# Performance work log

Hardware: AMD Instinct MI355X
Metric: run time of the kernel (lower is better)

Reference implementation:

```python
import jax, jax.numpy as jnp
import numpy as np


def setup_inputs() -> dict:
    key = jax.random.key(0)
    k1, k2 = jax.random.split(key)
    B, S, N, M = 4, 4, 4096, 4096
    output_points = jax.random.normal(k1, (B, S, N, 3), dtype=jnp.float32)
    target_points = jax.random.normal(k2, (B, S, M, 3), dtype=jnp.float32)
    return {"output_points": output_points, "target_points": target_points, "n_samples": 4096}


def reference(output_points, target_points, n_samples):
    # output_points: [B,S,N,3], target_points: [B,S,M,3] (already sampled to n_samples pts)
    x2 = jnp.sum(output_points * output_points, axis=-1)  # [B,S,N]
    y2 = jnp.sum(target_points * target_points, axis=-1)  # [B,S,M]
    xy = jnp.einsum('bsnd,bsmd->bsnm', output_points, target_points)  # [B,S,N,M]
    # squared pairwise distances; clamp tiny negatives from fp error
    d2 = jnp.maximum(x2[..., :, None] + y2[..., None, :] - 2.0 * xy, 0.0)
    dist1 = jnp.min(d2, axis=-1)  # [B,S,N] NN dist output->target (squared)
    dist2 = jnp.min(d2, axis=-2)  # [B,S,M] NN dist target->output (squared)
    # dist_combined per (b,s) = mean(dist1) + mean(dist2); tensor is [S,B]
    chamfer = jnp.mean(dist1, axis=-1) + jnp.mean(dist2, axis=-1)  # [B,S]
    return chamfer.T  # [n_future_steps, batch_size]
```

## Files before the change

### kernel.cpp

```cpp
#include <hip/hip_runtime.h>


constexpr int B = 4, S = 4, NPTS = 4096, PAIRS = B * S;
constexpr int UNITS = PAIRS * 2;
constexpr int THREADS = 512;
constexpr int WAVES = THREADS / 64;
constexpr int AFRAGS = 8;
constexpr int QPB = WAVES * AFRAGS * 16;
constexpr int QCH = NPTS / QPB;
constexpr int RCH = 4;
constexpr int RPB = NPTS / RCH;
constexpr int RTILES = RPB / 16;
constexpr unsigned short BF16_ONE = 0x3F80;

typedef __attribute__((ext_vector_type(8))) short bf16x8;
typedef __attribute__((ext_vector_type(4))) float f32x4;
typedef __attribute__((ext_vector_type(4))) unsigned int u32x4;

static __device__ inline unsigned short bf16_rne(float v) {
  unsigned int u = __builtin_bit_cast(unsigned int, v);
  u += 0x7FFFu + ((u >> 16) & 1u);
  return (unsigned short)(u >> 16);
}
static __device__ inline float bf16f(unsigned short h) {
  unsigned int u = (unsigned int)h << 16;
  return __builtin_bit_cast(float, u);
}
static __device__ inline unsigned int bpack(unsigned short lo, unsigned short hi) {
  return (unsigned int)lo | ((unsigned int)hi << 16);
}

struct Split3 { unsigned short h, m, l; };
static __device__ inline Split3 split3(float v) {
  Split3 s;
  s.h = bf16_rne(v);
  float r = v - bf16f(s.h);
  s.m = bf16_rne(r);
  r -= bf16f(s.m);
  s.l = bf16_rne(r);
  return s;
}


__global__ __launch_bounds__(THREADS, 4)
void chamfer_mfma_main(const float* __restrict__ out_pts,
                       const float* __restrict__ tgt_pts,
                       float* __restrict__ part) {
  const int t = threadIdx.x;
  const int l = t & 63;
  const int wid = t >> 6;
  const int qc = blockIdx.x;
  const int rc = blockIdx.y;
  const int unit = blockIdx.z;
  const int pair = unit >> 1, dir = unit & 1;

  const float* qpts = (dir == 0 ? out_pts : tgt_pts) + (size_t)pair * NPTS * 3;
  const float* rpts = (dir == 0 ? tgt_pts : out_pts) + (size_t)pair * NPTS * 3;

  __shared__ u32x4 lds[RTILES * 64];

  {
    const int q0 = qc * QPB;
    #pragma unroll
    for (int rep = 0; rep < QPB / THREADS; ++rep) {
      const int j = t + rep * THREADS;
      const float x = qpts[3 * (q0 + j)];
      const float y = qpts[3 * (q0 + j) + 1];
      const float z = qpts[3 * (q0 + j) + 2];
      const Split3 sx = split3(x), sy = split3(y), sz = split3(z);
      u32x4* base = lds + (j >> 4) * 64 + (j & 15);
      const u32x4 g0 = {bpack(sx.h, sx.h), bpack(sx.m, sx.h),
                        bpack(sx.l, sx.m), bpack(sy.h, sy.h)};
      const u32x4 g1 = {bpack(sy.m, sy.h), bpack(sy.l, sy.m),
                        bpack(sz.h, sz.h), bpack(sz.m, sz.h)};
      const u32x4 g2 = {bpack(sz.l, sz.m), bpack(BF16_ONE, BF16_ONE),
                        bpack(BF16_ONE, 0), 0u};
      const u32x4 g3 = {0u, 0u, 0u, 0u};
      base[0] = g0; base[16] = g1; base[32] = g2; base[48] = g3;
    }
  }
  __syncthreads();

  bf16x8 a[AFRAGS];
  #pragma unroll
  for (int m = 0; m < AFRAGS; ++m)
    a[m] = ((const bf16x8*)lds)[(wid * AFRAGS + m) * 64 + l];
  __syncthreads();

  {
    const int r0 = rc * RPB;
    #pragma unroll
    for (int rep = 0; rep < RPB / THREADS; ++rep) {
      const int j = t + rep * THREADS;
      const float x = rpts[3 * (r0 + j)];
      const float y = rpts[3 * (r0 + j) + 1];
      const float z = rpts[3 * (r0 + j) + 2];
      const float w = -0.5f * (x * x + y * y + z * z);
      const Split3 sx = split3(x), sy = split3(y), sz = split3(z), sw = split3(w);
      u32x4* base = lds + (j >> 4) * 64 + (j & 15);
      const u32x4 g0 = {bpack(sx.h, sx.m), bpack(sx.h, sx.l),
                        bpack(sx.h, sx.m), bpack(sy.h, sy.m)};
      const u32x4 g1 = {bpack(sy.h, sy.l), bpack(sy.h, sy.m),
                        bpack(sz.h, sz.m), bpack(sz.h, sz.l)};
      const u32x4 g2 = {bpack(sz.h, sz.m), bpack(sw.h, sw.m),
                        bpack(sw.l, 0), 0u};
      const u32x4 g3 = {0u, 0u, 0u, 0u};
      base[0] = g0; base[16] = g1; base[32] = g2; base[48] = g3;
    }
  }
  __syncthreads();

  f32x4 acc[AFRAGS];
  #pragma unroll
  for (int m = 0; m < AFRAGS; ++m)
    acc[m] = (f32x4){-3.0e38f, -3.0e38f, -3.0e38f, -3.0e38f};

  const f32x4 czero = {0.f, 0.f, 0.f, 0.f};
  const bf16x8* bptr = (const bf16x8*)lds;
  for (int tt = 0; tt < RTILES; tt += 2) {
    const bf16x8 b0 = bptr[tt * 64 + l];
    const bf16x8 b1 = bptr[(tt + 1) * 64 + l];
    #pragma unroll
    for (int m = 0; m < AFRAGS; ++m) {
      const f32x4 d0 = __builtin_amdgcn_mfma_f32_16x16x32_bf16(a[m], b0, czero, 0, 0, 0);
      const f32x4 d1 = __builtin_amdgcn_mfma_f32_16x16x32_bf16(a[m], b1, czero, 0, 0, 0);
      #pragma unroll
      for (int c = 0; c < 4; ++c)
        acc[m][c] = fmaxf(fmaxf(acc[m][c], d0[c]), d1[c]);
    }
  }

  #pragma unroll
  for (int m = 0; m < AFRAGS; ++m) {
    #pragma unroll
    for (int c = 0; c < 4; ++c) {
      float g = acc[m][c];
      g = fmaxf(g, __shfl_xor(g, 1, 64));
      g = fmaxf(g, __shfl_xor(g, 2, 64));
      g = fmaxf(g, __shfl_xor(g, 4, 64));
      g = fmaxf(g, __shfl_xor(g, 8, 64));
      acc[m][c] = g;
    }
  }
  const int jj = l & 15, hi = l >> 4;
  float v_lo = 0.f, v_hi = 0.f;
  #pragma unroll
  for (int m = 0; m < 4; ++m) {
    #pragma unroll
    for (int c = 0; c < 4; ++c) {
      const bool sel = (jj == m * 4 + c);
      v_lo = sel ? acc[m][c] : v_lo;
      v_hi = sel ? acc[m + 4][c] : v_hi;
    }
  }
  const int q = qc * QPB + wid * (AFRAGS * 16) + (jj >> 2) * 16 + hi * 4 + (jj & 3);
  float* pdst = part + ((size_t)unit * NPTS + q) * RCH + rc;
  pdst[0] = v_lo;
  pdst[64 * RCH] = v_hi;
}

__global__ __launch_bounds__(256)
void chamfer_finalize(const float* __restrict__ out_pts,
                      const float* __restrict__ tgt_pts,
                      const float* __restrict__ part,
                      float* __restrict__ out) {
  const int t = threadIdx.x;
  const int blk = blockIdx.x;
  const int unit = blk >> 4;
  const int q = (blk & 15) * 256 + t;
  const int pair = unit >> 1, dir = unit & 1;
  const float* qpts = (dir == 0 ? out_pts : tgt_pts) + (size_t)pair * NPTS * 3;

  const f32x4 p = *(const f32x4*)(part + ((size_t)unit * NPTS + q) * RCH);
  const float g = fmaxf(fmaxf(p[0], p[1]), fmaxf(p[2], p[3]));
  const float x = qpts[3 * q], y = qpts[3 * q + 1], z = qpts[3 * q + 2];
  const float x2 = x * x + y * y + z * z;
  float d = fmaxf(fmaf(-2.0f, g, x2), 0.0f);

  #pragma unroll
  for (int off = 1; off < 64; off <<= 1) d += __shfl_xor(d, off, 64);
  __shared__ float sum4[4];
  if ((t & 63) == 0) sum4[t >> 6] = d;
  __syncthreads();
  if (t == 0) {
    const float ssum = (sum4[0] + sum4[1]) + (sum4[2] + sum4[3]);
    const int b = pair >> 2, s = pair & 3;
    atomicAdd(&out[s * B + b], ssum * (1.0f / NPTS));
  }
}

extern "C" void kernel_launch(void* const* d_in, const int* in_sizes, int n_in,
                              void* d_out, int out_size, void* d_ws, size_t ws_size,
                              hipStream_t stream) {
  (void)in_sizes; (void)n_in; (void)ws_size;
  const float* out_pts = (const float*)d_in[0];
  const float* tgt_pts = (const float*)d_in[1];
  float* out = (float*)d_out;
  float* part = (float*)d_ws;

  hipMemsetAsync(out, 0, out_size * sizeof(float), stream);
  dim3 grid(QCH, RCH, UNITS);
  chamfer_mfma_main<<<grid, THREADS, 0, stream>>>(out_pts, tgt_pts, part);
  chamfer_finalize<<<dim3(UNITS * 16), 256, 0, stream>>>(out_pts, tgt_pts, part, out);
}
```

Measured before the change: 92.34 us.

## Fuse finalize into main chamfer kernel with in-block reference loop and prefetch

Result: faster. 87.10 us (-5.7%).

```diff
diff --git a/kernel.cpp b/kernel.cpp
--- a/kernel.cpp
+++ b/kernel.cpp
@@ -1,16 +1,13 @@
 #include <hip/hip_runtime.h>
 
 
-constexpr int B = 4, S = 4, NPTS = 4096, PAIRS = B * S;
-constexpr int UNITS = PAIRS * 2;
+constexpr int B = 4, S = 4, NPTS = 4096;
+constexpr int UNITS = B * S * 2;
 constexpr int THREADS = 512;
-constexpr int WAVES = THREADS / 64;
+constexpr int QPB = 512;
+constexpr int QCH = NPTS / QPB;
+constexpr int CHUNKS = 4;
 constexpr int AFRAGS = 8;
-constexpr int QPB = WAVES * AFRAGS * 16;
-constexpr int QCH = NPTS / QPB;
-constexpr int RCH = 4;
-constexpr int RPB = NPTS / RCH;
-constexpr int RTILES = RPB / 16;
 constexpr unsigned short BF16_ONE = 0x3F80;
 
 typedef __attribute__((ext_vector_type(8))) short bf16x8;
@@ -41,74 +38,64 @@
   return s;
 }
 
+static __device__ inline void write_arec(u32x4* lds, int rec,
+                                         float x, float y, float z) {
+  const Split3 sx = split3(x), sy = split3(y), sz = split3(z);
+  u32x4* base = lds + (rec >> 4) * 64 + (rec & 15);
+  base[0]  = (u32x4){bpack(sx.h, sx.h), bpack(sx.m, sx.h),
+                     bpack(sx.l, sx.m), bpack(sy.h, sy.h)};
+  base[16] = (u32x4){bpack(sy.m, sy.h), bpack(sy.l, sy.m),
+                     bpack(sz.h, sz.h), bpack(sz.m, sz.h)};
+  base[32] = (u32x4){bpack(sz.l, sz.m), bpack(BF16_ONE, BF16_ONE),
+                     bpack(BF16_ONE, 0), 0u};
+  base[48] = (u32x4){0u, 0u, 0u, 0u};
+}
+static __device__ inline void write_brec(u32x4* lds, int rec,
+                                         float x, float y, float z) {
+  const float w = -0.5f * (x * x + y * y + z * z);
+  const Split3 sx = split3(x), sy = split3(y), sz = split3(z), sw = split3(w);
+  u32x4* base = lds + (rec >> 4) * 64 + (rec & 15);
+  base[0]  = (u32x4){bpack(sx.h, sx.m), bpack(sx.h, sx.l),
+                     bpack(sx.h, sx.m), bpack(sy.h, sy.m)};
+  base[16] = (u32x4){bpack(sy.h, sy.l), bpack(sy.h, sy.m),
+                     bpack(sz.h, sz.m), bpack(sz.h, sz.l)};
+  base[32] = (u32x4){bpack(sz.h, sz.m), bpack(sw.h, sw.m),
+                     bpack(sw.l, 0), 0u};
+  base[48] = (u32x4){0u, 0u, 0u, 0u};
+}
 
-__global__ __launch_bounds__(THREADS, 4)
-void chamfer_mfma_main(const float* __restrict__ out_pts,
-                       const float* __restrict__ tgt_pts,
-                       float* __restrict__ part) {
+__global__ __launch_bounds__(THREADS, 2)
+void chamfer_fused(const float* __restrict__ out_pts,
+                   const float* __restrict__ tgt_pts,
+                   float* __restrict__ out) {
   const int t = threadIdx.x;
   const int l = t & 63;
   const int wid = t >> 6;
   const int qc = blockIdx.x;
-  const int rc = blockIdx.y;
-  const int unit = blockIdx.z;
+  const int unit = blockIdx.y;
   const int pair = unit >> 1, dir = unit & 1;
 
   const float* qpts = (dir == 0 ? out_pts : tgt_pts) + (size_t)pair * NPTS * 3;
   const float* rpts = (dir == 0 ? tgt_pts : out_pts) + (size_t)pair * NPTS * 3;
 
-  __shared__ u32x4 lds[RTILES * 64];
+  __shared__ u32x4 lds[64 * 64];
 
+  float x2;
   {
-    const int q0 = qc * QPB;
-    #pragma unroll
-    for (int rep = 0; rep < QPB / THREADS; ++rep) {
-      const int j = t + rep * THREADS;
-      const float x = qpts[3 * (q0 + j)];
-      const float y = qpts[3 * (q0 + j) + 1];
-      const float z = qpts[3 * (q0 + j) + 2];
-      const Split3 sx = split3(x), sy = split3(y), sz = split3(z);
-      u32x4* base = lds + (j >> 4) * 64 + (j & 15);
-      const u32x4 g0 = {bpack(sx.h, sx.h), bpack(sx.m, sx.h),
-                        bpack(sx.l, sx.m), bpack(sy.h, sy.h)};
-      const u32x4 g1 = {bpack(sy.m, sy.h), bpack(sy.l, sy.m),
-                        bpack(sz.h, sz.h), bpack(sz.m, sz.h)};
-      const u32x4 g2 = {bpack(sz.l, sz.m), bpack(BF16_ONE, BF16_ONE),
-                        bpack(BF16_ONE, 0), 0u};
-      const u32x4 g3 = {0u, 0u, 0u, 0u};
-      base[0] = g0; base[16] = g1; base[32] = g2; base[48] = g3;
-    }
+    const int q = qc * QPB + t;
+    const float x = qpts[3 * q], y = qpts[3 * q + 1], z = qpts[3 * q + 2];
+    x2 = x * x + y * y + z * z;
+    write_arec(lds, t, x, y, z);
   }
+
+  float nx0 = rpts[3 * t],            ny0 = rpts[3 * t + 1],            nz0 = rpts[3 * t + 2];
+  float nx1 = rpts[3 * (2048 + t)],   ny1 = rpts[3 * (2048 + t) + 1],   nz1 = rpts[3 * (2048 + t) + 2];
+
   __syncthreads();
-
   bf16x8 a[AFRAGS];
   #pragma unroll
   for (int m = 0; m < AFRAGS; ++m)
-    a[m] = ((const bf16x8*)lds)[(wid * AFRAGS + m) * 64 + l];
-  __syncthreads();
-
-  {
-    const int r0 = rc * RPB;
-    #pragma unroll
-    for (int rep = 0; rep < RPB / THREADS; ++rep) {
-      const int j = t + rep * THREADS;
-      const float x = rpts[3 * (r0 + j)];
-      const float y = rpts[3 * (r0 + j) + 1];
-      const float z = rpts[3 * (r0 + j) + 2];
-      const float w = -0.5f * (x * x + y * y + z * z);
-      const Split3 sx = split3(x), sy = split3(y), sz = split3(z), sw = split3(w);
-      u32x4* base = lds + (j >> 4) * 64 + (j & 15);
-      const u32x4 g0 = {bpack(sx.h, sx.m), bpack(sx.h, sx.l),
-                        bpack(sx.h, sx.m), bpack(sy.h, sy.m)};
-      const u32x4 g1 = {bpack(sy.h, sy.l), bpack(sy.h, sy.m),
-                        bpack(sz.h, sz.m), bpack(sz.h, sz.l)};
-      const u32x4 g2 = {bpack(sz.h, sz.m), bpack(sw.h, sw.m),
-                        bpack(sw.l, 0), 0u};
-      const u32x4 g3 = {0u, 0u, 0u, 0u};
-      base[0] = g0; base[16] = g1; base[32] = g2; base[48] = g3;
-    }
-  }
-  __syncthreads();
+    a[m] = ((const bf16x8*)lds)[((wid & 3) * AFRAGS + m) * 64 + l];
 
   f32x4 acc[AFRAGS];
   #pragma unroll
@@ -116,74 +103,75 @@
     acc[m] = (f32x4){-3.0e38f, -3.0e38f, -3.0e38f, -3.0e38f};
 
   const f32x4 czero = {0.f, 0.f, 0.f, 0.f};
-  const bf16x8* bptr = (const bf16x8*)lds;
-  for (int tt = 0; tt < RTILES; tt += 2) {
-    const bf16x8 b0 = bptr[tt * 64 + l];
-    const bf16x8 b1 = bptr[(tt + 1) * 64 + l];
-    #pragma unroll
-    for (int m = 0; m < AFRAGS; ++m) {
-      const f32x4 d0 = __builtin_amdgcn_mfma_f32_16x16x32_bf16(a[m], b0, czero, 0, 0, 0);
-      const f32x4 d1 = __builtin_amdgcn_mfma_f32_16x16x32_bf16(a[m], b1, czero, 0, 0, 0);
+  const int tb = (wid >> 2) * 32;
+  const bf16x8* bp = (const bf16x8*)lds;
+
+  for (int c = 0; c < CHUNKS; ++c) {
+    __syncthreads();
+    write_brec(lds, t,       nx0, ny0, nz0);
+    write_brec(lds, 512 + t, nx1, ny1, nz1);
+    __syncthreads();
+    if (c + 1 < CHUNKS) {
+      const int jlo = (c + 1) * 512 + t, jhi = 2048 + (c + 1) * 512 + t;
+      nx0 = rpts[3 * jlo]; ny0 = rpts[3 * jlo + 1]; nz0 = rpts[3 * jlo + 2];
+      nx1 = rpts[3 * jhi]; ny1 = rpts[3 * jhi + 1]; nz1 = rpts[3 * jhi + 2];
+    }
+    for (int tt = 0; tt < 32; tt += 2) {
+      const bf16x8 b0 = bp[(tb + tt) * 64 + l];
+      const bf16x8 b1 = bp[(tb + tt + 1) * 64 + l];
       #pragma unroll
-      for (int c = 0; c < 4; ++c)
-        acc[m][c] = fmaxf(fmaxf(acc[m][c], d0[c]), d1[c]);
+      for (int m = 0; m < AFRAGS; ++m) {
+        const f32x4 d0 = __builtin_amdgcn_mfma_f32_16x16x32_bf16(a[m], b0, czero, 0, 0, 0);
+        const f32x4 d1 = __builtin_amdgcn_mfma_f32_16x16x32_bf16(a[m], b1, czero, 0, 0, 0);
+        #pragma unroll
+        for (int k = 0; k < 4; ++k)
+          acc[m][k] = fmaxf(fmaxf(acc[m][k], d0[k]), d1[k]);
+      }
     }
   }
+
+  __syncthreads();
 
   #pragma unroll
   for (int m = 0; m < AFRAGS; ++m) {
     #pragma unroll
-    for (int c = 0; c < 4; ++c) {
-      float g = acc[m][c];
+    for (int k = 0; k < 4; ++k) {
+      float g = acc[m][k];
       g = fmaxf(g, __shfl_xor(g, 1, 64));
       g = fmaxf(g, __shfl_xor(g, 2, 64));
       g = fmaxf(g, __shfl_xor(g, 4, 64));
       g = fmaxf(g, __shfl_xor(g, 8, 64));
-      acc[m][c] = g;
+      acc[m][k] = g;
     }
   }
-  const int jj = l & 15, hi = l >> 4;
+  const int jj = l & 15, h = l >> 4;
   float v_lo = 0.f, v_hi = 0.f;
   #pragma unroll
   for (int m = 0; m < 4; ++m) {
     #pragma unroll
-    for (int c = 0; c < 4; ++c) {
-      const bool sel = (jj == m * 4 + c);
-      v_lo = sel ? acc[m][c] : v_lo;
-      v_hi = sel ? acc[m + 4][c] : v_hi;
+    for (int k = 0; k < 4; ++k) {
+      const bool sel = (jj == m * 4 + k);
+      v_lo = sel ? acc[m][k] : v_lo;
+      v_hi = sel ? acc[m + 4][k] : v_hi;
     }
   }
-  const int q = qc * QPB + wid * (AFRAGS * 16) + (jj >> 2) * 16 + hi * 4 + (jj & 3);
-  float* pdst = part + ((size_t)unit * NPTS + q) * RCH + rc;
-  pdst[0] = v_lo;
-  pdst[64 * RCH] = v_hi;
-}
+  float* Sg = reinterpret_cast<float*>(lds);
+  const int qloc = (wid & 3) * 128 + (jj >> 2) * 16 + h * 4 + (jj & 3);
+  Sg[(wid >> 2) * 512 + qloc] = v_lo;
+  Sg[(wid >> 2) * 512 + qloc + 64] = v_hi;
+  __syncthreads();
 
-__global__ __launch_bounds__(256)
-void chamfer_finalize(const float* __restrict__ out_pts,
-                      const float* __restrict__ tgt_pts,
-                      const float* __restrict__ part,
-                      float* __restrict__ out) {
-  const int t = threadIdx.x;
-  const int blk = blockIdx.x;
-  const int unit = blk >> 4;
-  const int q = (blk & 15) * 256 + t;
-  const int pair = unit >> 1, dir = unit & 1;
-  const float* qpts = (dir == 0 ? out_pts : tgt_pts) + (size_t)pair * NPTS * 3;
-
-  const f32x4 p = *(const f32x4*)(part + ((size_t)unit * NPTS + q) * RCH);
-  const float g = fmaxf(fmaxf(p[0], p[1]), fmaxf(p[2], p[3]));
-  const float x = qpts[3 * q], y = qpts[3 * q + 1], z = qpts[3 * q + 2];
-  const float x2 = x * x + y * y + z * z;
-  float d = fmaxf(fmaf(-2.0f, g, x2), 0.0f);
-
+  const float gq = fmaxf(Sg[t], Sg[512 + t]);
+  float d = fmaxf(fmaf(-2.0f, gq, x2), 0.0f);
   #pragma unroll
   for (int off = 1; off < 64; off <<= 1) d += __shfl_xor(d, off, 64);
-  __shared__ float sum4[4];
-  if ((t & 63) == 0) sum4[t >> 6] = d;
+  __syncthreads();
+  if (l == 0) Sg[wid] = d;
   __syncthreads();
   if (t == 0) {
-    const float ssum = (sum4[0] + sum4[1]) + (sum4[2] + sum4[3]);
+    float ssum = 0.f;
+    #pragma unroll
+    for (int w = 0; w < 8; ++w) ssum += Sg[w];
     const int b = pair >> 2, s = pair & 3;
     atomicAdd(&out[s * B + b], ssum * (1.0f / NPTS));
   }
@@ -192,14 +180,12 @@
 extern "C" void kernel_launch(void* const* d_in, const int* in_sizes, int n_in,
                               void* d_out, int out_size, void* d_ws, size_t ws_size,
                               hipStream_t stream) {
-  (void)in_sizes; (void)n_in; (void)ws_size;
+  (void)in_sizes; (void)n_in; (void)d_ws; (void)ws_size;
   const float* out_pts = (const float*)d_in[0];
   const float* tgt_pts = (const float*)d_in[1];
   float* out = (float*)d_out;
-  float* part = (float*)d_ws;
 
   hipMemsetAsync(out, 0, out_size * sizeof(float), stream);
-  dim3 grid(QCH, RCH, UNITS);
-  chamfer_mfma_main<<<grid, THREADS, 0, stream>>>(out_pts, tgt_pts, part);
-  chamfer_finalize<<<dim3(UNITS * 16), 256, 0, stream>>>(out_pts, tgt_pts, part, out);
+  dim3 grid(QCH, UNITS, 1);
+  chamfer_fused<<<grid, THREADS, 0, stream>>>(out_pts, tgt_pts, out);
 }
```
